# Optimization experiments

Measured on AMD Instinct MI355X. Metric: run time of the kernel, lower is better.

## Reference

```python
import jax, jax.numpy as jnp
import numpy as np

TEMPERATURE = 8.0  # sqrt(d_k) with d_k = 64


def setup_inputs() -> dict:
    key = jax.random.key(0)
    ks = jax.random.split(key, 5)
    shape = (64, 1024, 64)  # [B*H, N, d_k]
    return {
        "q": jax.random.normal(ks[0], shape, dtype=jnp.float32),
        "k": jax.random.normal(ks[1], shape, dtype=jnp.float32),
        "v": jax.random.normal(ks[2], shape, dtype=jnp.float32),
        "q_sem": jax.random.normal(ks[3], shape, dtype=jnp.float32),
        "k_sem": jax.random.normal(ks[4], shape, dtype=jnp.float32),
    }


def reference(q, k, v, q_sem, k_sem):
    # Semantic fusion branch (q_sem is not None): scores are recomputed
    # with the fused queries/keys. (The original also computes an unused
    # softmax over the pre-fusion scores and an unused attn_sem bmm --
    # dead code with no effect on outputs, so omitted.)
    qf = q + q_sem
    kf = k + k_sem
    attn_score = jnp.einsum("bnd,bmd->bnm", qf, kf) / TEMPERATURE  # [BH, N, N]
    attn = jax.nn.softmax(attn_score, axis=2)
    # dropout in eval mode == identity
    output = jnp.einsum("bnm,bmd->bnd", attn, v)  # [BH, N, d_k]
    return (output, attn, attn_score)
```

## Files before the change

kernel.cpp:

```cpp
#include <hip/hip_runtime.h>
#include <math.h>


#define BH 64
#define N 1024
#define D 64
#define TK 64
#define NC (N / TK)
#define KSTR 68
#define SSTR 68
#define LOG2E 1.44269504088896f
#define ESHIFT (-17.3123404907f)

typedef float    f32x4 __attribute__((ext_vector_type(4)));
typedef _Float16 half8 __attribute__((ext_vector_type(8)));
typedef _Float16 half4 __attribute__((ext_vector_type(4)));
typedef __fp16   fp16x2 __attribute__((ext_vector_type(2)));

__global__ __launch_bounds__(512, 4) void attn_fused_kernel(
    const float* __restrict__ q, const float* __restrict__ k,
    const float* __restrict__ v, const float* __restrict__ qs,
    const float* __restrict__ ks, float* __restrict__ out_o,
    float* __restrict__ out_a, float* __restrict__ out_s)
{
    __shared__ __align__(16) _Float16 Kb[TK][KSTR];
    __shared__ __align__(16) _Float16 Vt[D][KSTR];
    __shared__ __align__(16) float    Sst[32][SSTR];
    __shared__ float rsumf[32];

    const int t  = threadIdx.x;
    const int w  = t >> 6;
    const int l  = t & 63;
    const int lr = l & 15;
    const int lg = l >> 4;
    const int qt = w >> 2;
    const int kt = w & 3;

    const int wg = blockIdx.x;
    const int b  = ((wg >> 8) << 3) | (wg & 7);
    const int q0 = ((wg >> 3) & 31) * 32;

    const size_t inb = (size_t)b * (N * D);
    const size_t sb  = (size_t)b * N * N + (size_t)q0 * N;

    half8 qa[2];
    {
        const float* qp  = q  + inb + (size_t)(q0 + qt * 16 + lr) * D + lg * 8;
        const float* qsp = qs + inb + (size_t)(q0 + qt * 16 + lr) * D + lg * 8;
#pragma unroll
        for (int kst = 0; kst < 2; ++kst) {
            f32x4 a0 = *(const f32x4*)(qp + kst * 32);
            f32x4 a1 = *(const f32x4*)(qp + kst * 32 + 4);
            f32x4 c0 = *(const f32x4*)(qsp + kst * 32);
            f32x4 c1 = *(const f32x4*)(qsp + kst * 32 + 4);
            f32x4 s0 = a0 + c0, s1 = a1 + c1;
            union { half8 h8; fp16x2 h2[4]; } u;
            u.h2[0] = __builtin_amdgcn_cvt_pkrtz(s0[0], s0[1]);
            u.h2[1] = __builtin_amdgcn_cvt_pkrtz(s0[2], s0[3]);
            u.h2[2] = __builtin_amdgcn_cvt_pkrtz(s1[0], s1[1]);
            u.h2[3] = __builtin_amdgcn_cvt_pkrtz(s1[2], s1[3]);
            qa[kst] = u.h8;
        }
    }

    const int  ts = t & 255;
    const bool kstager = (w < 4);

    auto STAGE = [&](int kc) {
        if (kstager) {
            const f32x4* kbp = (const f32x4*)(k  + inb + (size_t)kc * TK * D);
            const f32x4* sbp = (const f32x4*)(ks + inb + (size_t)kc * TK * D);
#pragma unroll
            for (int h = 0; h < 2; ++h) {
                f32x4 k0 = kbp[(2 * h)     * 256 + ts];
                f32x4 k1 = kbp[(2 * h + 1) * 256 + ts];
                f32x4 s0 = sbp[(2 * h)     * 256 + ts];
                f32x4 s1 = sbp[(2 * h + 1) * 256 + ts];
                f32x4 m0 = k0 + s0, m1 = k1 + s1;
                const int row0 = (2 * h) * 16 + (ts >> 4);
                const int col  = (ts & 15) * 4;
                union { half4 h4; fp16x2 h2[2]; } u0, u1;
                u0.h2[0] = __builtin_amdgcn_cvt_pkrtz(m0[0], m0[1]);
                u0.h2[1] = __builtin_amdgcn_cvt_pkrtz(m0[2], m0[3]);
                u1.h2[0] = __builtin_amdgcn_cvt_pkrtz(m1[0], m1[1]);
                u1.h2[1] = __builtin_amdgcn_cvt_pkrtz(m1[2], m1[3]);
                *(half4*)&Kb[row0][col]      = u0.h4;
                *(half4*)&Kb[row0 + 16][col] = u1.h4;
            }
        } else {
            const f32x4* vbp = (const f32x4*)(v + inb + (size_t)kc * TK * D);
            f32x4 vr0 = vbp[((ts >> 4) * 4 + 0) * 16 + (ts & 15)];
            f32x4 vr1 = vbp[((ts >> 4) * 4 + 1) * 16 + (ts & 15)];
            f32x4 vr2 = vbp[((ts >> 4) * 4 + 2) * 16 + (ts & 15)];
            f32x4 vr3 = vbp[((ts >> 4) * 4 + 3) * 16 + (ts & 15)];
            const int br4 = (ts >> 4) * 4, bc4 = (ts & 15) * 4;
#pragma unroll
            for (int c = 0; c < 4; ++c) {
                union { half4 h4; fp16x2 h2[2]; } u;
                u.h2[0] = __builtin_amdgcn_cvt_pkrtz(vr0[c], vr1[c]);
                u.h2[1] = __builtin_amdgcn_cvt_pkrtz(vr2[c], vr3[c]);
                *(half4*)&Vt[bc4 + c][br4] = u.h4;
            }
        }
    };

    f32x4 oacc = {0.f, 0.f, 0.f, 0.f};
    float rs = 0.0f;

    for (int kc = 0; kc < NC; ++kc) {
        __syncthreads();
        STAGE(kc);
        __syncthreads();

        {
            half8 kb0 = *(const half8*)&Kb[kt * 16 + lr][lg * 8];
            half8 kb1 = *(const half8*)&Kb[kt * 16 + lr][32 + lg * 8];
            f32x4 ac = {0.f, 0.f, 0.f, 0.f};
            ac = __builtin_amdgcn_mfma_f32_16x16x32_f16(qa[0], kb0, ac, 0, 0, 0);
            ac = __builtin_amdgcn_mfma_f32_16x16x32_f16(qa[1], kb1, ac, 0, 0, 0);
#pragma unroll
            for (int r = 0; r < 4; ++r)
                Sst[qt * 16 + lg * 4 + r][kt * 16 + lr] = ac[r] * 0.125f;
        }
        __syncthreads();

        {
            f32x4 sv = *(const f32x4*)&Sst[t >> 4][(t & 15) * 4];
            *(f32x4*)(out_s + sb + (size_t)(t >> 4) * N + kc * TK + (t & 15) * 4) = sv;
        }

#pragma unroll
        for (int kst = 0; kst < 2; ++kst) {
            f32x4 s0 = *(const f32x4*)&Sst[qt * 16 + lr][kst * 32 + lg * 8];
            f32x4 s1 = *(const f32x4*)&Sst[qt * 16 + lr][kst * 32 + lg * 8 + 4];
            float e[8];
#pragma unroll
            for (int i = 0; i < 4; ++i) {
                e[i]     = __builtin_amdgcn_exp2f(__builtin_fmaf(s0[i], LOG2E, ESHIFT));
                e[i + 4] = __builtin_amdgcn_exp2f(__builtin_fmaf(s1[i], LOG2E, ESHIFT));
            }
            if (kt == 0)
                rs += ((e[0] + e[1]) + (e[2] + e[3])) + ((e[4] + e[5]) + (e[6] + e[7]));
            union { half8 h8; fp16x2 h2[4]; } u;
            u.h2[0] = __builtin_amdgcn_cvt_pkrtz(e[0], e[1]);
            u.h2[1] = __builtin_amdgcn_cvt_pkrtz(e[2], e[3]);
            u.h2[2] = __builtin_amdgcn_cvt_pkrtz(e[4], e[5]);
            u.h2[3] = __builtin_amdgcn_cvt_pkrtz(e[6], e[7]);
            half8 vb = *(const half8*)&Vt[kt * 16 + lr][kst * 32 + lg * 8];
            oacc = __builtin_amdgcn_mfma_f32_16x16x32_f16(u.h8, vb, oacc, 0, 0, 0);
        }
    }

    if (kt == 0) {
        rs += __shfl_xor(rs, 16);
        rs += __shfl_xor(rs, 32);
        if (l < 16) rsumf[qt * 16 + l] = rs;
    }
    __syncthreads();
    if (t < 32) rsumf[t] = 1.0f / rsumf[t];
    __syncthreads();

#pragma unroll
    for (int r = 0; r < 4; ++r)
        Sst[qt * 16 + lg * 4 + r][kt * 16 + lr] =
            oacc[r] * rsumf[qt * 16 + lg * 4 + r];
    __syncthreads();
    {
        f32x4 ov = *(const f32x4*)&Sst[t >> 4][(t & 15) * 4];
        __builtin_nontemporal_store(ov,
            (f32x4*)(out_o + inb + (size_t)(q0 + (t >> 4)) * D + (t & 15) * 4));
    }

    {
        const int   arow = t >> 4;
        const int   ac0  = (t & 15) * 4;
        const float iva  = rsumf[arow];
        const float* sp  = out_s + sb + (size_t)arow * N + ac0;
        float*       ap  = out_a + sb + (size_t)arow * N + ac0;
#pragma unroll 4
        for (int cb = 0; cb < NC; ++cb) {
            f32x4 sv = *(const f32x4*)(sp + cb * TK);
            f32x4 av;
#pragma unroll
            for (int i = 0; i < 4; ++i)
                av[i] = __builtin_amdgcn_exp2f(__builtin_fmaf(sv[i], LOG2E, ESHIFT)) * iva;
            __builtin_nontemporal_store(av, (f32x4*)(ap + cb * TK));
        }
    }
}

extern "C" void kernel_launch(void* const* d_in, const int* in_sizes, int n_in,
                              void* d_out, int out_size, void* d_ws, size_t ws_size,
                              hipStream_t stream) {
    const float* q  = (const float*)d_in[0];
    const float* k  = (const float*)d_in[1];
    const float* v  = (const float*)d_in[2];
    const float* qs = (const float*)d_in[3];
    const float* ks = (const float*)d_in[4];

    float* out_o = (float*)d_out;
    float* out_a = out_o + (size_t)BH * N * D;
    float* out_s = out_a + (size_t)BH * N * N;

    attn_fused_kernel<<<dim3(BH * (N / 32)), dim3(512), 0, stream>>>(
        q, k, v, qs, ks, out_o, out_a, out_s);
}
```

Baseline: 718.6 us.

## Keep scores in registers via transposed QK MFMA, drop LDS score staging

The QK^T product is computed with K as the A operand, so each lane ends up holding four consecutive key scores for one query. Those scores are stored straight to global memory, exponentiated in registers and fed directly as the A operand of 16x16x16 MFMAs against V. This removes the shared-memory score tile and one block barrier per key chunk. Each wave now accumulates a partial output over its own 16 keys for all 64 head dimensions. The partial outputs and row sums are combined at the end with LDS atomics in a buffer that reuses the K staging area. The trade-offs are less coalesced 16-byte score stores scattered across rows and an extra atomic reduction step in the epilogue.

```diff
diff --git a/kernel.cpp b/kernel.cpp
--- a/kernel.cpp
+++ b/kernel.cpp
@@ -8,7 +8,6 @@
 #define TK 64
 #define NC (N / TK)
 #define KSTR 68
-#define SSTR 68
 #define LOG2E 1.44269504088896f
 #define ESHIFT (-17.3123404907f)
 
@@ -25,8 +24,8 @@
 {
     __shared__ __align__(16) _Float16 Kb[TK][KSTR];
     __shared__ __align__(16) _Float16 Vt[D][KSTR];
-    __shared__ __align__(16) float    Sst[32][SSTR];
     __shared__ float rsumf[32];
+    float* Obuf = (float*)&Kb[0][0];
 
     const int t  = threadIdx.x;
     const int w  = t >> 6;
@@ -34,7 +33,7 @@
     const int lr = l & 15;
     const int lg = l >> 4;
     const int qt = w >> 2;
-    const int kt = w & 3;
+    const int kv = w & 3;
 
     const int wg = blockIdx.x;
     const int b  = ((wg >> 8) << 3) | (wg & 7);
@@ -104,7 +103,9 @@
         }
     };
 
-    f32x4 oacc = {0.f, 0.f, 0.f, 0.f};
+    f32x4 oacc[4];
+#pragma unroll
+    for (int dt = 0; dt < 4; ++dt) oacc[dt] = (f32x4){0.f, 0.f, 0.f, 0.f};
     float rs = 0.0f;
 
     for (int kc = 0; kc < NC; ++kc) {
@@ -112,63 +113,59 @@
         STAGE(kc);
         __syncthreads();
 
-        {
-            half8 kb0 = *(const half8*)&Kb[kt * 16 + lr][lg * 8];
-            half8 kb1 = *(const half8*)&Kb[kt * 16 + lr][32 + lg * 8];
-            f32x4 ac = {0.f, 0.f, 0.f, 0.f};
-            ac = __builtin_amdgcn_mfma_f32_16x16x32_f16(qa[0], kb0, ac, 0, 0, 0);
-            ac = __builtin_amdgcn_mfma_f32_16x16x32_f16(qa[1], kb1, ac, 0, 0, 0);
-#pragma unroll
-            for (int r = 0; r < 4; ++r)
-                Sst[qt * 16 + lg * 4 + r][kt * 16 + lr] = ac[r] * 0.125f;
-        }
-        __syncthreads();
-
-        {
-            f32x4 sv = *(const f32x4*)&Sst[t >> 4][(t & 15) * 4];
-            *(f32x4*)(out_s + sb + (size_t)(t >> 4) * N + kc * TK + (t & 15) * 4) = sv;
-        }
-
-#pragma unroll
-        for (int kst = 0; kst < 2; ++kst) {
-            f32x4 s0 = *(const f32x4*)&Sst[qt * 16 + lr][kst * 32 + lg * 8];
-            f32x4 s1 = *(const f32x4*)&Sst[qt * 16 + lr][kst * 32 + lg * 8 + 4];
-            float e[8];
-#pragma unroll
-            for (int i = 0; i < 4; ++i) {
-                e[i]     = __builtin_amdgcn_exp2f(__builtin_fmaf(s0[i], LOG2E, ESHIFT));
-                e[i + 4] = __builtin_amdgcn_exp2f(__builtin_fmaf(s1[i], LOG2E, ESHIFT));
-            }
-            if (kt == 0)
-                rs += ((e[0] + e[1]) + (e[2] + e[3])) + ((e[4] + e[5]) + (e[6] + e[7]));
-            union { half8 h8; fp16x2 h2[4]; } u;
-            u.h2[0] = __builtin_amdgcn_cvt_pkrtz(e[0], e[1]);
-            u.h2[1] = __builtin_amdgcn_cvt_pkrtz(e[2], e[3]);
-            u.h2[2] = __builtin_amdgcn_cvt_pkrtz(e[4], e[5]);
-            u.h2[3] = __builtin_amdgcn_cvt_pkrtz(e[6], e[7]);
-            half8 vb = *(const half8*)&Vt[kt * 16 + lr][kst * 32 + lg * 8];
-            oacc = __builtin_amdgcn_mfma_f32_16x16x32_f16(u.h8, vb, oacc, 0, 0, 0);
-        }
-    }
-
-    if (kt == 0) {
-        rs += __shfl_xor(rs, 16);
-        rs += __shfl_xor(rs, 32);
-        if (l < 16) rsumf[qt * 16 + l] = rs;
-    }
+        half8 ka0 = *(const half8*)&Kb[kv * 16 + lr][lg * 8];
+        half8 ka1 = *(const half8*)&Kb[kv * 16 + lr][32 + lg * 8];
+        f32x4 ac = {0.f, 0.f, 0.f, 0.f};
+        ac = __builtin_amdgcn_mfma_f32_16x16x32_f16(ka0, qa[0], ac, 0, 0, 0);
+        ac = __builtin_amdgcn_mfma_f32_16x16x32_f16(ka1, qa[1], ac, 0, 0, 0);
+        f32x4 sv = { ac[0] * 0.125f, ac[1] * 0.125f,
+                     ac[2] * 0.125f, ac[3] * 0.125f };
+
+        *(f32x4*)(out_s + sb + (size_t)(qt * 16 + lr) * N
+                  + kc * TK + kv * 16 + lg * 4) = sv;
+
+        float e0 = __builtin_amdgcn_exp2f(__builtin_fmaf(sv[0], LOG2E, ESHIFT));
+        float e1 = __builtin_amdgcn_exp2f(__builtin_fmaf(sv[1], LOG2E, ESHIFT));
+        float e2 = __builtin_amdgcn_exp2f(__builtin_fmaf(sv[2], LOG2E, ESHIFT));
+        float e3 = __builtin_amdgcn_exp2f(__builtin_fmaf(sv[3], LOG2E, ESHIFT));
+        rs += (e0 + e1) + (e2 + e3);
+        union { half4 h4; fp16x2 h2[2]; } up;
+        up.h2[0] = __builtin_amdgcn_cvt_pkrtz(e0, e1);
+        up.h2[1] = __builtin_amdgcn_cvt_pkrtz(e2, e3);
+        const half4 pa = up.h4;
+
+#pragma unroll
+        for (int dt = 0; dt < 4; ++dt) {
+            half4 vb = *(const half4*)&Vt[dt * 16 + lr][kv * 16 + lg * 4];
+            oacc[dt] = __builtin_amdgcn_mfma_f32_16x16x16f16(pa, vb, oacc[dt], 0, 0, 0);
+        }
+    }
+
+    __syncthreads();
+    for (int i = t; i < 32 * 68; i += 512) Obuf[i] = 0.0f;
+    if (t < 32) rsumf[t] = 0.0f;
+    __syncthreads();
+
+    rs += __shfl_xor(rs, 16);
+    rs += __shfl_xor(rs, 32);
+    if (l < 16) atomicAdd(&rsumf[qt * 16 + l], rs);
+
+#pragma unroll
+    for (int dt = 0; dt < 4; ++dt)
+#pragma unroll
+    for (int r = 0; r < 4; ++r)
+        atomicAdd(&Obuf[(qt * 16 + lg * 4 + r) * 68 + dt * 16 + lr], oacc[dt][r]);
     __syncthreads();
     if (t < 32) rsumf[t] = 1.0f / rsumf[t];
     __syncthreads();
 
-#pragma unroll
-    for (int r = 0; r < 4; ++r)
-        Sst[qt * 16 + lg * 4 + r][kt * 16 + lr] =
-            oacc[r] * rsumf[qt * 16 + lg * 4 + r];
-    __syncthreads();
     {
-        f32x4 ov = *(const f32x4*)&Sst[t >> 4][(t & 15) * 4];
-        __builtin_nontemporal_store(ov,
-            (f32x4*)(out_o + inb + (size_t)(q0 + (t >> 4)) * D + (t & 15) * 4));
+        const int qo = t >> 4, doo = (t & 15) * 4;
+        f32x4 ov = *(const f32x4*)&Obuf[qo * 68 + doo];
+        const float iv = rsumf[qo];
+        f32x4 o2 = { ov[0] * iv, ov[1] * iv, ov[2] * iv, ov[3] * iv };
+        __builtin_nontemporal_store(o2,
+            (f32x4*)(out_o + inb + (size_t)(q0 + qo) * D + doo));
     }
 
     {
```

Measured after the change: 808.0 us. +12.4%, slower.

## Double query tile per block to reuse staged K/V across 64 rows

Applied to the files above, without the earlier changes.

Each workgroup now handles 64 query rows instead of 32, with each wave computing two 16-row query subtiles against the same staged K and V tiles. This halves the number of blocks and the global K/K_sem/V loading and fp16 conversion per query row, amortizing staging and barrier costs. In exchange each thread holds more registers (two Q fragments, two accumulators), shared memory for the score tile doubles, and the grid has fewer blocks, which may reduce occupancy or parallelism. The kernel is mostly bound by writing the two 256MB score and attention outputs, so the gain may be limited.

```diff
diff --git a/kernel.cpp b/kernel.cpp
--- a/kernel.cpp
+++ b/kernel.cpp
@@ -5,6 +5,7 @@
 #define BH 64
 #define N 1024
 #define D 64
+#define TM 64
 #define TK 64
 #define NC (N / TK)
 #define KSTR 68
@@ -19,14 +20,14 @@
 
 __global__ __launch_bounds__(512, 4) void attn_fused_kernel(
     const float* __restrict__ q, const float* __restrict__ k,
-    const float* __restrict__ v, const float* __restrict__ qs,
+    const float* __restrict__ v, const float* __restrict__ qsem,
     const float* __restrict__ ks, float* __restrict__ out_o,
     float* __restrict__ out_a, float* __restrict__ out_s)
 {
     __shared__ __align__(16) _Float16 Kb[TK][KSTR];
     __shared__ __align__(16) _Float16 Vt[D][KSTR];
-    __shared__ __align__(16) float    Sst[32][SSTR];
-    __shared__ float rsumf[32];
+    __shared__ __align__(16) float    Sst[TM][SSTR];
+    __shared__ float rsumf[TM];
 
     const int t  = threadIdx.x;
     const int w  = t >> 6;
@@ -37,16 +38,17 @@
     const int kt = w & 3;
 
     const int wg = blockIdx.x;
-    const int b  = ((wg >> 8) << 3) | (wg & 7);
-    const int q0 = ((wg >> 3) & 31) * 32;
+    const int b  = ((wg >> 7) << 3) | (wg & 7);
+    const int q0 = ((wg >> 3) & 15) * TM;
 
     const size_t inb = (size_t)b * (N * D);
     const size_t sb  = (size_t)b * N * N + (size_t)q0 * N;
 
-    half8 qa[2];
-    {
-        const float* qp  = q  + inb + (size_t)(q0 + qt * 16 + lr) * D + lg * 8;
-        const float* qsp = qs + inb + (size_t)(q0 + qt * 16 + lr) * D + lg * 8;
+    half8 qa[2][2];
+#pragma unroll
+    for (int qs = 0; qs < 2; ++qs) {
+        const float* qp  = q    + inb + (size_t)(q0 + (qt * 2 + qs) * 16 + lr) * D + lg * 8;
+        const float* qsp = qsem + inb + (size_t)(q0 + (qt * 2 + qs) * 16 + lr) * D + lg * 8;
 #pragma unroll
         for (int kst = 0; kst < 2; ++kst) {
             f32x4 a0 = *(const f32x4*)(qp + kst * 32);
@@ -59,7 +61,7 @@
             u.h2[1] = __builtin_amdgcn_cvt_pkrtz(s0[2], s0[3]);
             u.h2[2] = __builtin_amdgcn_cvt_pkrtz(s1[0], s1[1]);
             u.h2[3] = __builtin_amdgcn_cvt_pkrtz(s1[2], s1[3]);
-            qa[kst] = u.h8;
+            qa[qs][kst] = u.h8;
         }
     }
 
@@ -104,8 +106,10 @@
         }
     };
 
-    f32x4 oacc = {0.f, 0.f, 0.f, 0.f};
-    float rs = 0.0f;
+    f32x4 oacc[2];
+    oacc[0] = (f32x4){0.f, 0.f, 0.f, 0.f};
+    oacc[1] = (f32x4){0.f, 0.f, 0.f, 0.f};
+    float rs[2] = {0.f, 0.f};
 
     for (int kc = 0; kc < NC; ++kc) {
         __syncthreads();
@@ -115,64 +119,85 @@
         {
             half8 kb0 = *(const half8*)&Kb[kt * 16 + lr][lg * 8];
             half8 kb1 = *(const half8*)&Kb[kt * 16 + lr][32 + lg * 8];
-            f32x4 ac = {0.f, 0.f, 0.f, 0.f};
-            ac = __builtin_amdgcn_mfma_f32_16x16x32_f16(qa[0], kb0, ac, 0, 0, 0);
-            ac = __builtin_amdgcn_mfma_f32_16x16x32_f16(qa[1], kb1, ac, 0, 0, 0);
-#pragma unroll
-            for (int r = 0; r < 4; ++r)
-                Sst[qt * 16 + lg * 4 + r][kt * 16 + lr] = ac[r] * 0.125f;
+#pragma unroll
+            for (int qs = 0; qs < 2; ++qs) {
+                f32x4 ac = {0.f, 0.f, 0.f, 0.f};
+                ac = __builtin_amdgcn_mfma_f32_16x16x32_f16(qa[qs][0], kb0, ac, 0, 0, 0);
+                ac = __builtin_amdgcn_mfma_f32_16x16x32_f16(qa[qs][1], kb1, ac, 0, 0, 0);
+#pragma unroll
+                for (int r = 0; r < 4; ++r)
+                    Sst[(qt * 2 + qs) * 16 + lg * 4 + r][kt * 16 + lr] = ac[r] * 0.125f;
+            }
         }
         __syncthreads();
 
-        {
-            f32x4 sv = *(const f32x4*)&Sst[t >> 4][(t & 15) * 4];
-            *(f32x4*)(out_s + sb + (size_t)(t >> 4) * N + kc * TK + (t & 15) * 4) = sv;
+#pragma unroll
+        for (int h = 0; h < 2; ++h) {
+            const int srow = h * 32 + (t >> 4);
+            f32x4 sv = *(const f32x4*)&Sst[srow][(t & 15) * 4];
+            *(f32x4*)(out_s + sb + (size_t)srow * N + kc * TK + (t & 15) * 4) = sv;
         }
 
 #pragma unroll
         for (int kst = 0; kst < 2; ++kst) {
-            f32x4 s0 = *(const f32x4*)&Sst[qt * 16 + lr][kst * 32 + lg * 8];
-            f32x4 s1 = *(const f32x4*)&Sst[qt * 16 + lr][kst * 32 + lg * 8 + 4];
-            float e[8];
-#pragma unroll
-            for (int i = 0; i < 4; ++i) {
-                e[i]     = __builtin_amdgcn_exp2f(__builtin_fmaf(s0[i], LOG2E, ESHIFT));
-                e[i + 4] = __builtin_amdgcn_exp2f(__builtin_fmaf(s1[i], LOG2E, ESHIFT));
-            }
-            if (kt == 0)
-                rs += ((e[0] + e[1]) + (e[2] + e[3])) + ((e[4] + e[5]) + (e[6] + e[7]));
-            union { half8 h8; fp16x2 h2[4]; } u;
-            u.h2[0] = __builtin_amdgcn_cvt_pkrtz(e[0], e[1]);
-            u.h2[1] = __builtin_amdgcn_cvt_pkrtz(e[2], e[3]);
-            u.h2[2] = __builtin_amdgcn_cvt_pkrtz(e[4], e[5]);
-            u.h2[3] = __builtin_amdgcn_cvt_pkrtz(e[6], e[7]);
             half8 vb = *(const half8*)&Vt[kt * 16 + lr][kst * 32 + lg * 8];
-            oacc = __builtin_amdgcn_mfma_f32_16x16x32_f16(u.h8, vb, oacc, 0, 0, 0);
+#pragma unroll
+            for (int qs = 0; qs < 2; ++qs) {
+                const int prow = (qt * 2 + qs) * 16 + lr;
+                f32x4 s0 = *(const f32x4*)&Sst[prow][kst * 32 + lg * 8];
+                f32x4 s1 = *(const f32x4*)&Sst[prow][kst * 32 + lg * 8 + 4];
+                float e0 = __builtin_amdgcn_exp2f(__builtin_fmaf(s0[0], LOG2E, ESHIFT));
+                float e1 = __builtin_amdgcn_exp2f(__builtin_fmaf(s0[1], LOG2E, ESHIFT));
+                float e2 = __builtin_amdgcn_exp2f(__builtin_fmaf(s0[2], LOG2E, ESHIFT));
+                float e3 = __builtin_amdgcn_exp2f(__builtin_fmaf(s0[3], LOG2E, ESHIFT));
+                float e4 = __builtin_amdgcn_exp2f(__builtin_fmaf(s1[0], LOG2E, ESHIFT));
+                float e5 = __builtin_amdgcn_exp2f(__builtin_fmaf(s1[1], LOG2E, ESHIFT));
+                float e6 = __builtin_amdgcn_exp2f(__builtin_fmaf(s1[2], LOG2E, ESHIFT));
+                float e7 = __builtin_amdgcn_exp2f(__builtin_fmaf(s1[3], LOG2E, ESHIFT));
+                if (kt == 0)
+                    rs[qs] += ((e0 + e1) + (e2 + e3)) + ((e4 + e5) + (e6 + e7));
+                union { half8 h8; fp16x2 h2[4]; } u;
+                u.h2[0] = __builtin_amdgcn_cvt_pkrtz(e0, e1);
+                u.h2[1] = __builtin_amdgcn_cvt_pkrtz(e2, e3);
+                u.h2[2] = __builtin_amdgcn_cvt_pkrtz(e4, e5);
+                u.h2[3] = __builtin_amdgcn_cvt_pkrtz(e6, e7);
+                oacc[qs] = __builtin_amdgcn_mfma_f32_16x16x32_f16(u.h8, vb, oacc[qs], 0, 0, 0);
+            }
         }
     }
 
     if (kt == 0) {
-        rs += __shfl_xor(rs, 16);
-        rs += __shfl_xor(rs, 32);
-        if (l < 16) rsumf[qt * 16 + l] = rs;
+#pragma unroll
+        for (int qs = 0; qs < 2; ++qs) {
+            float x = rs[qs];
+            x += __shfl_xor(x, 16);
+            x += __shfl_xor(x, 32);
+            if (l < 16) rsumf[(qt * 2 + qs) * 16 + l] = x;
+        }
     }
     __syncthreads();
-    if (t < 32) rsumf[t] = 1.0f / rsumf[t];
+    if (t < TM) rsumf[t] = 1.0f / rsumf[t];
     __syncthreads();
 
 #pragma unroll
-    for (int r = 0; r < 4; ++r)
-        Sst[qt * 16 + lg * 4 + r][kt * 16 + lr] =
-            oacc[r] * rsumf[qt * 16 + lg * 4 + r];
+    for (int qs = 0; qs < 2; ++qs)
+#pragma unroll
+    for (int r = 0; r < 4; ++r) {
+        const int row = (qt * 2 + qs) * 16 + lg * 4 + r;
+        Sst[row][kt * 16 + lr] = oacc[qs][r] * rsumf[row];
+    }
     __syncthreads();
-    {
-        f32x4 ov = *(const f32x4*)&Sst[t >> 4][(t & 15) * 4];
+#pragma unroll
+    for (int h = 0; h < 2; ++h) {
+        const int srow = h * 32 + (t >> 4);
+        f32x4 ov = *(const f32x4*)&Sst[srow][(t & 15) * 4];
         __builtin_nontemporal_store(ov,
-            (f32x4*)(out_o + inb + (size_t)(q0 + (t >> 4)) * D + (t & 15) * 4));
-    }
-
-    {
-        const int   arow = t >> 4;
+            (f32x4*)(out_o + inb + (size_t)(q0 + srow) * D + (t & 15) * 4));
+    }
+
+#pragma unroll
+    for (int h = 0; h < 2; ++h) {
+        const int   arow = h * 32 + (t >> 4);
         const int   ac0  = (t & 15) * 4;
         const float iva  = rsumf[arow];
         const float* sp  = out_s + sb + (size_t)arow * N + ac0;
@@ -202,6 +227,6 @@
     float* out_a = out_o + (size_t)BH * N * D;
     float* out_s = out_a + (size_t)BH * N * N;
 
-    attn_fused_kernel<<<dim3(BH * (N / 32)), dim3(512), 0, stream>>>(
+    attn_fused_kernel<<<dim3(BH * (N / TM)), dim3(512), 0, stream>>>(
         q, k, v, qs, ks, out_o, out_a, out_s);
 }
```

Measured after the change: 690.3 us. -3.9%, faster.
